# Kernel optimization log

Measured on AMD Instinct MI355X. Metric: run time of the kernel, lower is better.

## Reference

```python
import jax, jax.numpy as jnp
import numpy as np

# Parameter-slice layout (baked from init_kwargs).
N_GROUPS = 4
# (kernel_group, col_start, col_end) for optimized parameter groups
OPT_SLICES = [(0, 0, 1024), (1, 1024, 2048), (2, 2048, 3072)]
# (prior_variance, col_start, col_end) for non-optimized params -> last group
NON_OPT_SLICES = [(1.0, 3072, 3584), (0.5, 3584, 4096)]

N_ROW, N_COL, P = 4096, 4096, 4096


def setup_inputs() -> dict:
    key = jax.random.key(0)
    k1, k2 = jax.random.split(key)
    J_row = jax.random.normal(k1, (N_ROW, P), dtype=jnp.float32)
    J_col = jax.random.normal(k2, (N_COL, P), dtype=jnp.float32)
    return {"J_row": J_row, "J_col": J_col}


def reference(J_row, J_col):
    # kernel_slice: [G, N_row, N_col]; each group accumulates J_row[:, s] @ J_col[:, s]^T
    kernel = jnp.zeros((N_GROUPS, J_row.shape[0], J_col.shape[0]), dtype=jnp.float32)
    for g, s0, s1 in OPT_SLICES:
        kernel = kernel.at[g].add(
            jnp.einsum('ij,kj->ik', J_row[:, s0:s1], J_col[:, s0:s1]))
    for pvar, s0, s1 in NON_OPT_SLICES:
        # with_prior_prec=True: scale contribution by prior variance pvar
        kernel = kernel.at[N_GROUPS - 1].add(
            jnp.float32(pvar) * jnp.einsum('ij,kj->ik', J_row[:, s0:s1], J_col[:, s0:s1]))
    return kernel
```

## Files before the change

kernel.cpp:

```cpp
#include <hip/hip_runtime.h>


typedef unsigned short ushort_t;
typedef __bf16 bf16x8 __attribute__((ext_vector_type(8)));
typedef float floatx4 __attribute__((ext_vector_type(4)));
typedef unsigned short ushortx8 __attribute__((ext_vector_type(8)));

#define PDIM 4096
#define BM 256
#define BN 256
#define BK 32
#define NBUF 4
#define BUFE 16384
#define NT 128
#define GT 32
#define KTSZ (PDIM * BK)

__device__ __forceinline__ unsigned short f2bf_rne(float f) {
  union { float f; unsigned u; } v; v.f = f;
  unsigned u = v.u;
  unsigned r = u + 0x7FFFu + ((u >> 16) & 1u);
  return (unsigned short)(r >> 16);
}

__global__ void convert_pack(const float* __restrict__ srcA,
                             const float* __restrict__ srcB,
                             ushort_t* __restrict__ dst) {
  const int mat = blockIdx.y;
  const float* src = mat ? srcB : srcA;
  const int kt = blockIdx.x & 127;
  const int mb = blockIdx.x >> 7;
  const int r = threadIdx.x >> 2;
  const int s = threadIdx.x & 3;
  const int row = mb * 64 + r;
  const float sc = (mat && kt >= 112) ? 0.5f : 1.0f;

  const float* p = src + (size_t)row * PDIM + kt * 32 + s * 8;
  float4 x = *(const float4*)p;
  float4 y = *(const float4*)(p + 4);
  ushortx8 o;
  o[0] = f2bf_rne(x.x * sc); o[1] = f2bf_rne(x.y * sc);
  o[2] = f2bf_rne(x.z * sc); o[3] = f2bf_rne(x.w * sc);
  o[4] = f2bf_rne(y.x * sc); o[5] = f2bf_rne(y.y * sc);
  o[6] = f2bf_rne(y.z * sc); o[7] = f2bf_rne(y.w * sc);

  const int slot = s ^ ((row >> 1) & 3);
  ushort_t* q = dst + (size_t)mat * PDIM * PDIM + (size_t)kt * KTSZ +
                row * 32 + slot * 8;
  *(ushortx8*)q = o;
}

__device__ __forceinline__ void async_copy16(const ushort_t* g, ushort_t* l) {
  __builtin_amdgcn_global_load_lds(
      (const __attribute__((address_space(1))) unsigned int*)(g),
      (__attribute__((address_space(3))) unsigned int*)(l),
      16, 0, 0);
}

__global__ __launch_bounds__(512, 2) void gemm_grouped(
    const ushort_t* __restrict__ P, float* __restrict__ out) {
  __shared__ ushort_t lds[NBUF * BUFE];

  const int tid = threadIdx.x;
  const int wave = tid >> 6;
  const int lane = tid & 63;
  const int m16 = lane & 15;
  const int quad = lane >> 4;
  const int wm = wave >> 2;
  const int wn = wave & 3;

  const int bid = blockIdx.x;
  const int xcd = bid & 7;
  const int loc = bid >> 3;
  const int tm = (xcd >> 1) * 4 + (loc >> 3);
  const int tn = (xcd & 1) * 8 + (loc & 7);
  const int row0 = tm * BM;
  const int col0 = tn * BN;

  unsigned goff[4];
  int lbase[4];
#pragma unroll
  for (int s = 0; s < 4; ++s) {
    int ch = wave * 4 + s;
    int isB = ch >> 4;
    int chloc = ch & 15;
    goff[s] = (unsigned)isB * (unsigned)(PDIM * PDIM) +
              (unsigned)((isB ? col0 : row0) * 32 + chloc * 512 + lane * 8);
    lbase[s] = isB * 8192 + chloc * 512;
  }

  int a_off[8], b_off[4];
  const int ksl = (quad ^ ((m16 >> 1) & 3)) * 8;
#pragma unroll
  for (int i = 0; i < 8; ++i)
    a_off[i] = (wm * 128 + i * 16 + m16) * 32 + ksl;
#pragma unroll
  for (int j = 0; j < 4; ++j)
    b_off[j] = 8192 + (wn * 64 + j * 16 + m16) * 32 + ksl;

  const int orow0 = row0 + wm * 128 + quad * 4;
  const int ocol0 = col0 + wn * 64 + m16;

  floatx4 acc[8][4];
#pragma unroll
  for (int i = 0; i < 8; ++i)
#pragma unroll
    for (int j = 0; j < 4; ++j)
      acc[i][j] = (floatx4){0.f, 0.f, 0.f, 0.f};

  auto stage = [&](int t) {
    const ushort_t* gbase = P + (size_t)t * KTSZ;
    int lb = (t & (NBUF - 1)) * BUFE;
#pragma unroll
    for (int s = 0; s < 4; ++s)
      async_copy16(gbase + goff[s], &lds[lb + lbase[s]]);
  };

  stage(0); stage(1); stage(2);
  asm volatile("s_waitcnt vmcnt(8)" ::: "memory");
  __builtin_amdgcn_s_barrier();

  for (int t = 0; t < NT; ++t) {
    if (t + 3 < NT) stage(t + 3);

    const ushort_t* lb = &lds[(t & (NBUF - 1)) * BUFE];
    bf16x8 af[8], bf[4];
#pragma unroll
    for (int i = 0; i < 8; ++i) af[i] = *(const bf16x8*)(lb + a_off[i]);
#pragma unroll
    for (int j = 0; j < 4; ++j) bf[j] = *(const bf16x8*)(lb + b_off[j]);

    __builtin_amdgcn_s_setprio(1);
#pragma unroll
    for (int i = 0; i < 8; ++i)
#pragma unroll
      for (int j = 0; j < 4; ++j)
        acc[i][j] = __builtin_amdgcn_mfma_f32_16x16x32_bf16(
            af[i], bf[j], acc[i][j], 0, 0, 0);
    __builtin_amdgcn_s_setprio(0);

    if (t < NT - 3)       asm volatile("s_waitcnt vmcnt(8)" ::: "memory");
    else if (t == NT - 3) asm volatile("s_waitcnt vmcnt(4)" ::: "memory");
    else                  asm volatile("s_waitcnt vmcnt(0)" ::: "memory");
    __builtin_amdgcn_s_barrier();

    if (((t + 1) & (GT - 1)) == 0) {
      const int g = t >> 5;
      float* outp = out + (size_t)g * PDIM * PDIM;
#pragma unroll
      for (int i = 0; i < 8; ++i)
#pragma unroll
        for (int j = 0; j < 4; ++j) {
#pragma unroll
          for (int v = 0; v < 4; ++v)
            outp[(size_t)(orow0 + i * 16 + v) * PDIM + (ocol0 + j * 16)] =
                acc[i][j][v];
          acc[i][j] = (floatx4){0.f, 0.f, 0.f, 0.f};
        }
    }
  }
}

extern "C" void kernel_launch(void* const* d_in, const int* in_sizes, int n_in,
                              void* d_out, int out_size, void* d_ws, size_t ws_size,
                              hipStream_t stream) {
  const float* J_row = (const float*)d_in[0];
  const float* J_col = (const float*)d_in[1];
  float* out = (float*)d_out;

  ushort_t* P = (ushort_t*)d_ws;

  dim3 cgrid(128 * 64, 2);
  convert_pack<<<cgrid, 256, 0, stream>>>(J_row, J_col, P);

  gemm_grouped<<<dim3(256), 512, 0, stream>>>(P, out);
}
```

Before: 467.2 us.

## Split GEMM k-step into four phases interleaving LDS reads, async loads, MFMA

Restructures the main loop into two k-tiles per iteration, each split into four sub-phases. Each phase loads a subset of A/B fragments from LDS, issues one async global-to-LDS copy, then runs an 8-MFMA block between barriers, in a ping-pong style schedule. The aim is to spread global loads and LDS reads across the compute so memory latency hides behind MFMA and register pressure drops. It adds many more workgroup barriers per k-tile, which may cost more in synchronisation than the overlap saves.

```diff
diff --git a/kernel.cpp b/kernel.cpp
--- a/kernel.cpp
+++ b/kernel.cpp
@@ -57,6 +57,30 @@
       16, 0, 0);
 }
 
+#define PHASE(LB, QA, QB, ST, SS, LOADA)                                     \
+  do {                                                                       \
+    if (LOADA) {                                                             \
+      _Pragma("unroll")                                                      \
+      for (int i = 0; i < 4; ++i)                                            \
+        af[i] = *(const bf16x8*)((LB) + a_off[(QA) * 4 + i]);                \
+    }                                                                        \
+    _Pragma("unroll")                                                        \
+    for (int j = 0; j < 2; ++j)                                              \
+      bfr[j] = *(const bf16x8*)((LB) + b_off[(QB) * 2 + j]);                 \
+    stage1((ST), (SS));                                                      \
+    __builtin_amdgcn_s_barrier();                                            \
+    asm volatile("s_waitcnt lgkmcnt(0)" ::: "memory");                       \
+    __builtin_amdgcn_s_setprio(1);                                           \
+    _Pragma("unroll")                                                        \
+    for (int i = 0; i < 4; ++i)                                              \
+      _Pragma("unroll")                                                      \
+      for (int j = 0; j < 2; ++j)                                            \
+        acc[(QA) * 4 + i][(QB) * 2 + j] =                                    \
+            __builtin_amdgcn_mfma_f32_16x16x32_bf16(                         \
+                af[i], bfr[j], acc[(QA) * 4 + i][(QB) * 2 + j], 0, 0, 0);    \
+    __builtin_amdgcn_s_setprio(0);                                           \
+  } while (0)
+
 __global__ __launch_bounds__(512, 2) void gemm_grouped(
     const ushort_t* __restrict__ P, float* __restrict__ out) {
   __shared__ ushort_t lds[NBUF * BUFE];
@@ -108,44 +132,53 @@
     for (int j = 0; j < 4; ++j)
       acc[i][j] = (floatx4){0.f, 0.f, 0.f, 0.f};
 
-  auto stage = [&](int t) {
-    const ushort_t* gbase = P + (size_t)t * KTSZ;
-    int lb = (t & (NBUF - 1)) * BUFE;
+  auto stage1 = [&](int t, int s) {
+    if (t < NT)
+      async_copy16(P + (size_t)t * KTSZ + goff[s],
+                   &lds[(t & (NBUF - 1)) * BUFE + lbase[s]]);
+  };
+  auto stage_all = [&](int t) {
 #pragma unroll
     for (int s = 0; s < 4; ++s)
-      async_copy16(gbase + goff[s], &lds[lb + lbase[s]]);
+      async_copy16(P + (size_t)t * KTSZ + goff[s],
+                   &lds[(t & (NBUF - 1)) * BUFE + lbase[s]]);
   };
 
-  stage(0); stage(1); stage(2);
+  stage_all(0); stage_all(1); stage_all(2);
   asm volatile("s_waitcnt vmcnt(8)" ::: "memory");
   __builtin_amdgcn_s_barrier();
 
-  for (int t = 0; t < NT; ++t) {
-    if (t + 3 < NT) stage(t + 3);
-
-    const ushort_t* lb = &lds[(t & (NBUF - 1)) * BUFE];
-    bf16x8 af[8], bf[4];
-#pragma unroll
-    for (int i = 0; i < 8; ++i) af[i] = *(const bf16x8*)(lb + a_off[i]);
-#pragma unroll
-    for (int j = 0; j < 4; ++j) bf[j] = *(const bf16x8*)(lb + b_off[j]);
-
-    __builtin_amdgcn_s_setprio(1);
-#pragma unroll
-    for (int i = 0; i < 8; ++i)
-#pragma unroll
-      for (int j = 0; j < 4; ++j)
-        acc[i][j] = __builtin_amdgcn_mfma_f32_16x16x32_bf16(
-            af[i], bf[j], acc[i][j], 0, 0, 0);
-    __builtin_amdgcn_s_setprio(0);
-
-    if (t < NT - 3)       asm volatile("s_waitcnt vmcnt(8)" ::: "memory");
-    else if (t == NT - 3) asm volatile("s_waitcnt vmcnt(4)" ::: "memory");
-    else                  asm volatile("s_waitcnt vmcnt(0)" ::: "memory");
-    __builtin_amdgcn_s_barrier();
-
-    if (((t + 1) & (GT - 1)) == 0) {
-      const int g = t >> 5;
+  for (int tp = 0; tp < NT / 2; ++tp) {
+    const int t0 = tp * 2;
+    const ushort_t* lb0 = &lds[(t0 & (NBUF - 1)) * BUFE];
+    const ushort_t* lb1 = &lds[((t0 + 1) & (NBUF - 1)) * BUFE];
+    bf16x8 af[4], bfr[2];
+
+    PHASE(lb0, 0, 0, t0 + 3, 0, true);
+    __builtin_amdgcn_s_barrier();
+    PHASE(lb0, 0, 1, t0 + 3, 1, false);
+    __builtin_amdgcn_s_barrier();
+    PHASE(lb0, 1, 0, t0 + 3, 2, true);
+    __builtin_amdgcn_s_barrier();
+    PHASE(lb0, 1, 1, t0 + 3, 3, false);
+    if (tp <= 62) asm volatile("s_waitcnt vmcnt(8)" ::: "memory");
+    else          asm volatile("s_waitcnt vmcnt(0)" ::: "memory");
+    __builtin_amdgcn_s_barrier();
+
+    PHASE(lb1, 0, 0, t0 + 4, 0, true);
+    __builtin_amdgcn_s_barrier();
+    PHASE(lb1, 0, 1, t0 + 4, 1, false);
+    __builtin_amdgcn_s_barrier();
+    PHASE(lb1, 1, 0, t0 + 4, 2, true);
+    __builtin_amdgcn_s_barrier();
+    PHASE(lb1, 1, 1, t0 + 4, 3, false);
+    if (tp <= 61)      asm volatile("s_waitcnt vmcnt(8)" ::: "memory");
+    else if (tp == 62) asm volatile("s_waitcnt vmcnt(4)" ::: "memory");
+    else               asm volatile("s_waitcnt vmcnt(0)" ::: "memory");
+    __builtin_amdgcn_s_barrier();
+
+    if (((t0 + 2) & (GT - 1)) == 0) {
+      const int g = (t0 + 1) >> 5;
       float* outp = out + (size_t)g * PDIM * PDIM;
 #pragma unroll
       for (int i = 0; i < 8; ++i)
```

Result: no change. 474.6 us (+1.6%).
